# Kernel tuning notes

Hardware: AMD Instinct MI355X
Metric: run time of the kernel (lower is better)

## Reference

```python
import jax, jax.numpy as jnp
import numpy as np

N_NODES = 50000
N_EDGES = 600000
N_GRAPHS = 256


def gcn_conv(x, W, b, src, dst, n):
    # PyG GCNConv: out = D^{-1/2} (A + I) D^{-1/2} X W + b
    h = x @ W  # [N, out]
    deg = jax.ops.segment_sum(jnp.ones((src.shape[0],), h.dtype), dst, num_segments=n) + 1.0  # self-loop
    dinv = jax.lax.rsqrt(deg)  # deg >= 1 so safe
    msgs = h[src] * (dinv[src] * dinv[dst])[:, None]  # [E, out]
    agg = jax.ops.segment_sum(msgs, dst, num_segments=n)
    agg = agg + h * (dinv * dinv)[:, None]  # self-loop contribution
    return agg + b


def setup_inputs() -> dict:
    key = jax.random.key(0)
    ks = jax.random.split(key, 8)
    x = jax.random.normal(ks[0], (N_NODES, 1), dtype=jnp.float32)
    edge_index = jax.random.randint(ks[1], (2, N_EDGES), 0, N_NODES, dtype=jnp.int64)
    batch = jnp.sort(jax.random.randint(ks[2], (N_NODES,), 0, N_GRAPHS, dtype=jnp.int64))

    def glorot(k, shape):
        lim = np.sqrt(6.0 / (shape[0] + shape[1]))
        return jax.random.uniform(k, shape, jnp.float32, -lim, lim)

    return {
        "x": x,
        "W1": glorot(ks[3], (1, 64)), "b1": jnp.zeros((64,), jnp.float32),
        "W2": glorot(ks[4], (64, 128)), "b2": jnp.zeros((128,), jnp.float32),
        "W3": glorot(ks[5], (128, 64)), "b3": jnp.zeros((64,), jnp.float32),
        "lin1_w": glorot(ks[6], (64, 32)), "lin1_b": jnp.zeros((32,), jnp.float32),
        "lin2_w": glorot(ks[7], (32, 1)), "lin2_b": jnp.zeros((1,), jnp.float32),
        "edge_index": edge_index,
        "batch": batch,
    }


def reference(x, W1, b1, W2, b2, W3, b3, lin1_w, lin1_b, lin2_w, lin2_b, edge_index, batch):
    src, dst = edge_index[0], edge_index[1]
    n = x.shape[0]
    h = jax.nn.relu(gcn_conv(x, W1, b1, src, dst, n))
    h = jax.nn.relu(gcn_conv(h, W2, b2, src, dst, n))
    h = jax.nn.relu(gcn_conv(h, W3, b3, src, dst, n))
    # global_mean_pool
    sums = jax.ops.segment_sum(h, batch, num_segments=N_GRAPHS)
    cnts = jax.ops.segment_sum(jnp.ones((n,), h.dtype), batch, num_segments=N_GRAPHS)
    pooled = sums / jnp.maximum(cnts, 1.0)[:, None]  # [G, 64]
    z = jax.nn.relu(pooled @ lin1_w + lin1_b)
    return z @ lin2_w + lin2_b  # [G, 1]
```

## Files before the change

kernel.cpp:

```cpp
#include <hip/hip_runtime.h>
#include <hip/hip_fp16.h>


#define N_FEAT 64
#define POOL_SUB 16
#define SLOT 64

typedef _Float16 f16x4 __attribute__((ext_vector_type(4)));
typedef float f32x4 __attribute__((ext_vector_type(4)));

__global__ void fill_kernel(const int* __restrict__ src, const int* __restrict__ dst,
                            int* __restrict__ deg, int* __restrict__ csr, int E) {
    int e4 = (blockIdx.x * blockDim.x + threadIdx.x) * 4;
    if (e4 + 3 < E) {
        int4 sv = *(const int4*)&src[e4];
        int4 dv = *(const int4*)&dst[e4];
        int p0 = atomicAdd(&deg[dv.x], 1);
        int p1 = atomicAdd(&deg[dv.y], 1);
        int p2 = atomicAdd(&deg[dv.z], 1);
        int p3 = atomicAdd(&deg[dv.w], 1);
        csr[dv.x * SLOT + p0] = sv.x;
        csr[dv.y * SLOT + p1] = sv.y;
        csr[dv.z * SLOT + p2] = sv.z;
        csr[dv.w * SLOT + p3] = sv.w;
    } else {
        for (int e = e4; e < E; ++e) {
            int d = dst[e];
            int pos = atomicAdd(&deg[d], 1);
            csr[d * SLOT + pos] = src[e];
        }
    }
}

__global__ void prep_kernel(const int* __restrict__ deg, const float* __restrict__ x,
                            float* __restrict__ dinv, float* __restrict__ xd,
                            const float* __restrict__ W2, const float* __restrict__ W3,
                            __half* __restrict__ W2p, __half* __restrict__ W3p, int N) {
    int i = blockIdx.x * blockDim.x + threadIdx.x;
    if (i < N) {
        float dv = rsqrtf((float)deg[i] + 1.0f);
        dinv[i] = dv;
        xd[i] = x[i] * dv;
    }
    if (i < 16384) {
        if (i < 8192) {
            int ii = i & 3;
            int lane = (i >> 2) & 63;
            int blk = i >> 8;
            int k = (blk & 3) * 16 + (lane >> 4) * 4 + ii;
            int col = (blk >> 2) * 16 + (lane & 15);
            W2p[i] = __float2half(W2[k * 128 + col]);
        } else {
            int t2 = i - 8192;
            int ii = t2 & 3;
            int lane = (t2 >> 2) & 63;
            int blk = t2 >> 8;
            int k = (blk & 7) * 16 + (lane >> 4) * 4 + ii;
            int col = (blk >> 3) * 16 + (lane & 15);
            W3p[t2] = __float2half(W3[k * 64 + col]);
        }
    }
}

__global__ void sagg_gather(const int* __restrict__ deg, const int* __restrict__ csr,
                            const float* __restrict__ xd, const float* __restrict__ dinv,
                            float2* __restrict__ sd, int N) {
    int wid = (blockIdx.x * blockDim.x + threadIdx.x) >> 6;
    int lane = threadIdx.x & 63;
    int v = wid * 4 + (lane >> 4);
    int sub = lane & 15;
    if (v >= N) return;
    int dg = deg[v];
    int base = v * SLOT;
    float sum = 0.0f;
    for (int j = sub; j < dg; j += 16) sum += xd[csr[base + j]];
    #pragma unroll
    for (int off = 8; off; off >>= 1) sum += __shfl_xor(sum, off);
    if (sub == 0) {
        float dv = dinv[v];
        sd[v] = make_float2(dv * (sum + xd[v]), dv);
    }
}

__global__ void agg1_gather(const int* __restrict__ deg, const int* __restrict__ csr,
                            const float2* __restrict__ sd,
                            const float* __restrict__ W1, const float* __restrict__ b1,
                            __half* __restrict__ agg16, int N) {
    int wave = (blockIdx.x * blockDim.x + threadIdx.x) >> 6;
    int lane = threadIdx.x & 63;
    int v = wave * 2 + (lane >> 5);
    int sub = lane & 31;
    if (v >= N) return;
    float2 w  = *(const float2*)&W1[sub * 2];
    float2 bb = *(const float2*)&b1[sub * 2];
    int dg = deg[v];
    int base = v * SLOT;
    float ax = 0.0f, ay = 0.0f;
    int j = 0;
    for (; j + 3 < dg; j += 4) {
        int4 u = *(const int4*)&csr[base + j];
        float2 p0 = sd[u.x];
        float2 p1 = sd[u.y];
        float2 p2 = sd[u.z];
        float2 p3 = sd[u.w];
        ax += fmaxf(p0.x * w.x + bb.x, 0.0f) * p0.y + fmaxf(p1.x * w.x + bb.x, 0.0f) * p1.y;
        ax += fmaxf(p2.x * w.x + bb.x, 0.0f) * p2.y + fmaxf(p3.x * w.x + bb.x, 0.0f) * p3.y;
        ay += fmaxf(p0.x * w.y + bb.y, 0.0f) * p0.y + fmaxf(p1.x * w.y + bb.y, 0.0f) * p1.y;
        ay += fmaxf(p2.x * w.y + bb.y, 0.0f) * p2.y + fmaxf(p3.x * w.y + bb.y, 0.0f) * p3.y;
    }
    for (; j < dg; ++j) {
        float2 p = sd[csr[base + j]];
        ax += fmaxf(p.x * w.x + bb.x, 0.0f) * p.y;
        ay += fmaxf(p.x * w.y + bb.y, 0.0f) * p.y;
    }
    float2 pv = sd[v];
    float dv = pv.y;
    float ox = dv * ax + fmaxf(pv.x * w.x + bb.x, 0.0f) * dv * dv;
    float oy = dv * ay + fmaxf(pv.x * w.y + bb.y, 0.0f) * dv * dv;
    *(__half2*)&agg16[(size_t)v * N_FEAT + sub * 2] = __floats2half2_rn(ox, oy);
}

#define H2PAD 136
__global__ __launch_bounds__(256) void gemm12(const __half* __restrict__ A16,
                                              const __half* __restrict__ W2p,
                                              const float* __restrict__ bias2,
                                              const __half* __restrict__ W3p,
                                              const float* __restrict__ dinv,
                                              __half* __restrict__ md, int M) {
    __shared__ __half h2s[32 * H2PAD];
    int tid = threadIdx.x;
    int wave = tid >> 6, lane = tid & 63;
    int g = lane >> 4, r = lane & 15;
    int row0 = blockIdx.x * 32;

    f16x4 af[2][4];
    #pragma unroll
    for (int rt = 0; rt < 2; ++rt) {
        int row = row0 + rt * 16 + r;
        if (row >= M) row = M - 1;
        const __half* ap = A16 + (size_t)row * 64 + g * 4;
        #pragma unroll
        for (int kc = 0; kc < 4; ++kc)
            af[rt][kc] = *(const f16x4*)(ap + kc * 16);
    }

    f32x4 acc[2][2] = {};
    const f16x4* w2v = (const f16x4*)W2p;
    #pragma unroll
    for (int ctl = 0; ctl < 2; ++ctl) {
        int ct = wave * 2 + ctl;
        #pragma unroll
        for (int kc = 0; kc < 4; ++kc) {
            f16x4 bf = w2v[(ct * 4 + kc) * 64 + lane];
            acc[0][ctl] = __builtin_amdgcn_mfma_f32_16x16x16f16(af[0][kc], bf, acc[0][ctl], 0, 0, 0);
            acc[1][ctl] = __builtin_amdgcn_mfma_f32_16x16x16f16(af[1][kc], bf, acc[1][ctl], 0, 0, 0);
        }
    }
    #pragma unroll
    for (int ctl = 0; ctl < 2; ++ctl) {
        int col = (wave * 2 + ctl) * 16 + r;
        float bb = bias2[col];
        #pragma unroll
        for (int rt = 0; rt < 2; ++rt)
            #pragma unroll
            for (int i = 0; i < 4; ++i)
                h2s[(rt * 16 + g * 4 + i) * H2PAD + col] =
                    __float2half(fmaxf(acc[rt][ctl][i] + bb, 0.f));
    }
    __syncthreads();

    f32x4 acc2[2] = {};
    const f16x4* w3v = (const f16x4*)W3p;
    #pragma unroll
    for (int kc = 0; kc < 8; ++kc) {
        f16x4 bf = w3v[(wave * 8 + kc) * 64 + lane];
        #pragma unroll
        for (int rt = 0; rt < 2; ++rt) {
            f16x4 a2 = *(const f16x4*)&h2s[(rt * 16 + r) * H2PAD + kc * 16 + g * 4];
            acc2[rt] = __builtin_amdgcn_mfma_f32_16x16x16f16(a2, bf, acc2[rt], 0, 0, 0);
        }
    }
    #pragma unroll
    for (int rt = 0; rt < 2; ++rt)
        #pragma unroll
        for (int i = 0; i < 4; ++i) {
            int row = row0 + rt * 16 + g * 4 + i;
            if (row < M)
                md[(size_t)row * 64 + wave * 16 + r] = __float2half(acc2[rt][i] * dinv[row]);
        }
}

__global__ void agg3_gather(const int* __restrict__ deg, const int* __restrict__ csr,
                            const __half* __restrict__ md, const float* __restrict__ dinv,
                            float* __restrict__ agg, int N) {
    int wave = (blockIdx.x * blockDim.x + threadIdx.x) >> 6;
    int lane = threadIdx.x & 63;
    int v = wave * 4 + (lane >> 4);
    int sub = lane & 15;
    if (v >= N) return;
    const uint2* mdp = (const uint2*)md;
    int dg = deg[v];
    int base = v * SLOT;
    uint2 sv = mdp[(size_t)v * 16 + sub];
    float2 f0 = __half22float2(*(const __half2*)&sv.x);
    float2 f1 = __half22float2(*(const __half2*)&sv.y);
    float a0 = f0.x, a1 = f0.y, a2 = f1.x, a3 = f1.y;
    int j = 0;
    for (; j + 3 < dg; j += 4) {
        int4 u = *(const int4*)&csr[base + j];
        uint2 x0 = mdp[(size_t)u.x * 16 + sub];
        uint2 x1 = mdp[(size_t)u.y * 16 + sub];
        uint2 x2 = mdp[(size_t)u.z * 16 + sub];
        uint2 x3 = mdp[(size_t)u.w * 16 + sub];
        float2 p0 = __half22float2(*(const __half2*)&x0.x), q0 = __half22float2(*(const __half2*)&x0.y);
        float2 p1 = __half22float2(*(const __half2*)&x1.x), q1 = __half22float2(*(const __half2*)&x1.y);
        float2 p2 = __half22float2(*(const __half2*)&x2.x), q2 = __half22float2(*(const __half2*)&x2.y);
        float2 p3 = __half22float2(*(const __half2*)&x3.x), q3 = __half22float2(*(const __half2*)&x3.y);
        a0 += (p0.x + p1.x) + (p2.x + p3.x);
        a1 += (p0.y + p1.y) + (p2.y + p3.y);
        a2 += (q0.x + q1.x) + (q2.x + q3.x);
        a3 += (q0.y + q1.y) + (q2.y + q3.y);
    }
    for (; j < dg; ++j) {
        uint2 xv = mdp[(size_t)csr[base + j] * 16 + sub];
        float2 t0 = __half22float2(*(const __half2*)&xv.x);
        float2 t1 = __half22float2(*(const __half2*)&xv.y);
        a0 += t0.x; a1 += t0.y; a2 += t1.x; a3 += t1.y;
    }
    float dv = dinv[v];
    *(float4*)&agg[(size_t)v * N_FEAT + sub * 4] =
        make_float4(a0 * dv, a1 * dv, a2 * dv, a3 * dv);
}

__global__ void pool_kernel(const float* __restrict__ agg, const float* __restrict__ b3,
                            const int* __restrict__ batch, float* __restrict__ pooled,
                            float* __restrict__ counts, int N) {
    int wave = (blockIdx.x * blockDim.x + threadIdx.x) >> 6;
    int lane = threadIdx.x & 63;
    int start = wave * POOL_SUB;
    if (start >= N) return;
    int end = min(start + POOL_SUB, N);
    float bl = b3[lane];
    int cur = batch[start];
    float acc = 0.0f;
    float cnt = 0.0f;
    for (int i = start; i < end; ++i) {
        int g = batch[i];
        if (g != cur) {
            atomicAdd(&pooled[cur * N_FEAT + lane], acc);
            if (lane == 0) atomicAdd(&counts[cur], cnt);
            acc = 0.0f; cnt = 0.0f; cur = g;
        }
        acc += fmaxf(agg[(size_t)i * N_FEAT + lane] + bl, 0.0f);
        cnt += 1.0f;
    }
    atomicAdd(&pooled[cur * N_FEAT + lane], acc);
    if (lane == 0) atomicAdd(&counts[cur], cnt);
}

__global__ void mlp_kernel(const float* __restrict__ pooled, const float* __restrict__ counts,
                           const float* __restrict__ l1w, const float* __restrict__ l1b,
                           const float* __restrict__ l2w, const float* __restrict__ l2b,
                           float* __restrict__ out) {
    __shared__ float row[64];
    __shared__ float zs[32];
    int g = blockIdx.x;
    int l = threadIdx.x;
    float cnt = fmaxf(counts[g], 1.0f);
    row[l] = pooled[g * 64 + l] / cnt;
    __syncthreads();
    if (l < 32) {
        float z = l1b[l];
        #pragma unroll
        for (int k = 0; k < 64; ++k) z += row[k] * l1w[k * 32 + l];
        zs[l] = fmaxf(z, 0.0f);
    }
    __syncthreads();
    if (l == 0) {
        float o = l2b[0];
        #pragma unroll
        for (int j = 0; j < 32; ++j) o += zs[j] * l2w[j];
        out[g] = o;
    }
}

extern "C" void kernel_launch(void* const* d_in, const int* in_sizes, int n_in,
                              void* d_out, int out_size, void* d_ws, size_t ws_size,
                              hipStream_t stream) {
    const float* x   = (const float*)d_in[0];
    const float* W1  = (const float*)d_in[1];
    const float* b1  = (const float*)d_in[2];
    const float* W2  = (const float*)d_in[3];
    const float* b2  = (const float*)d_in[4];
    const float* W3  = (const float*)d_in[5];
    const float* b3  = (const float*)d_in[6];
    const float* l1w = (const float*)d_in[7];
    const float* l1b = (const float*)d_in[8];
    const float* l2w = (const float*)d_in[9];
    const float* l2b = (const float*)d_in[10];
    const int* ei    = (const int*)d_in[11];
    const int* batch = (const int*)d_in[12];

    int N = in_sizes[0];
    int E = in_sizes[11] / 2;
    int G = out_size;
    const int* src = ei;
    const int* dst = ei + E;

    char* wsb = (char*)d_ws;
    int*   deg      = (int*)wsb;                 wsb += (size_t)N * 4;
    float* pooled   = (float*)wsb;               wsb += (size_t)G * 64 * 4;
    float* counts   = (float*)wsb;               wsb += (size_t)G * 4;
    int*   csr      = (int*)wsb;                 wsb += (size_t)N * SLOT * 4;
    float* dinv     = (float*)wsb;               wsb += (size_t)N * 4;
    float* xd       = (float*)wsb;               wsb += (size_t)N * 4;
    float2* sd      = (float2*)wsb;              wsb += (size_t)N * 8;
    float* agg      = (float*)wsb;               wsb += (size_t)N * 64 * 4;
    __half* md      = (__half*)wsb;              wsb += (size_t)N * 64 * 2;
    __half* agg16   = (__half*)wsb;              wsb += ((size_t)N + 32) * 64 * 2;
    __half* W2p     = (__half*)wsb;              wsb += 8192 * 2;
    __half* W3p     = (__half*)wsb;              wsb += 8192 * 2;

    hipMemsetAsync(deg, 0, ((size_t)N + (size_t)G * 64 + G) * 4, stream);

    int tb = 256;
    fill_kernel<<<(E / 4 + tb - 1) / tb, tb, 0, stream>>>(src, dst, deg, csr, E);
    prep_kernel<<<(N + tb - 1) / tb, tb, 0, stream>>>(deg, x, dinv, xd, W2, W3, W2p, W3p, N);
    sagg_gather<<<((N + 3) / 4 + 3) / 4, tb, 0, stream>>>(deg, csr, xd, dinv, sd, N);
    int a1_waves = (N + 1) / 2;
    agg1_gather<<<(a1_waves + 3) / 4, tb, 0, stream>>>(deg, csr, sd, W1, b1, agg16, N);
    gemm12<<<(N + 31) / 32, tb, 0, stream>>>(agg16, W2p, b2, W3p, dinv, md, N);
    int a3_waves = (N + 3) / 4;
    agg3_gather<<<(a3_waves + 3) / 4, tb, 0, stream>>>(deg, csr, md, dinv, agg, N);
    int pool_waves = (N + POOL_SUB - 1) / POOL_SUB;
    pool_kernel<<<(pool_waves + 3) / 4, tb, 0, stream>>>(agg, b3, batch, pooled, counts, N);
    mlp_kernel<<<G, 64, 0, stream>>>(pooled, counts, l1w, l1b, l2w, l2b, (float*)d_out);
}
```

Before: 196.7 us.

## Fuse layer-3 aggregation with bias, ReLU and mean-pool via wave-level atomics

Merges the final GCN gather kernel with the pooling kernel. Bias and ReLU are applied in registers, and the four nodes handled by a wave are reduced with shuffles when they share a graph before atomically adding into the pooled buffer. This removes the N×64 fp32 agg round trip through memory and one kernel launch. In exchange it issues many more atomics per node than the old 16-node-per-wave pooling, which could cause contention on the 256 graph rows.

```diff
diff --git a/kernel.cpp b/kernel.cpp
--- a/kernel.cpp
+++ b/kernel.cpp
@@ -3,7 +3,6 @@
 
 
 #define N_FEAT 64
-#define POOL_SUB 16
 #define SLOT 64
 
 typedef _Float16 f16x4 __attribute__((ext_vector_type(4)));
@@ -190,72 +189,73 @@
         }
 }
 
-__global__ void agg3_gather(const int* __restrict__ deg, const int* __restrict__ csr,
-                            const __half* __restrict__ md, const float* __restrict__ dinv,
-                            float* __restrict__ agg, int N) {
+__global__ void agg3_pool(const int* __restrict__ deg, const int* __restrict__ csr,
+                          const __half* __restrict__ md, const float* __restrict__ dinv,
+                          const float* __restrict__ b3, const int* __restrict__ batch,
+                          float* __restrict__ pooled, float* __restrict__ counts, int N) {
     int wave = (blockIdx.x * blockDim.x + threadIdx.x) >> 6;
     int lane = threadIdx.x & 63;
-    int v = wave * 4 + (lane >> 4);
+    int qw = lane >> 4;
+    int v = wave * 4 + qw;
     int sub = lane & 15;
-    if (v >= N) return;
-    const uint2* mdp = (const uint2*)md;
-    int dg = deg[v];
-    int base = v * SLOT;
-    uint2 sv = mdp[(size_t)v * 16 + sub];
-    float2 f0 = __half22float2(*(const __half2*)&sv.x);
-    float2 f1 = __half22float2(*(const __half2*)&sv.y);
-    float a0 = f0.x, a1 = f0.y, a2 = f1.x, a3 = f1.y;
-    int j = 0;
-    for (; j + 3 < dg; j += 4) {
-        int4 u = *(const int4*)&csr[base + j];
-        uint2 x0 = mdp[(size_t)u.x * 16 + sub];
-        uint2 x1 = mdp[(size_t)u.y * 16 + sub];
-        uint2 x2 = mdp[(size_t)u.z * 16 + sub];
-        uint2 x3 = mdp[(size_t)u.w * 16 + sub];
-        float2 p0 = __half22float2(*(const __half2*)&x0.x), q0 = __half22float2(*(const __half2*)&x0.y);
-        float2 p1 = __half22float2(*(const __half2*)&x1.x), q1 = __half22float2(*(const __half2*)&x1.y);
-        float2 p2 = __half22float2(*(const __half2*)&x2.x), q2 = __half22float2(*(const __half2*)&x2.y);
-        float2 p3 = __half22float2(*(const __half2*)&x3.x), q3 = __half22float2(*(const __half2*)&x3.y);
-        a0 += (p0.x + p1.x) + (p2.x + p3.x);
-        a1 += (p0.y + p1.y) + (p2.y + p3.y);
-        a2 += (q0.x + q1.x) + (q2.x + q3.x);
-        a3 += (q0.y + q1.y) + (q2.y + q3.y);
-    }
-    for (; j < dg; ++j) {
-        uint2 xv = mdp[(size_t)csr[base + j] * 16 + sub];
-        float2 t0 = __half22float2(*(const __half2*)&xv.x);
-        float2 t1 = __half22float2(*(const __half2*)&xv.y);
-        a0 += t0.x; a1 += t0.y; a2 += t1.x; a3 += t1.y;
-    }
-    float dv = dinv[v];
-    *(float4*)&agg[(size_t)v * N_FEAT + sub * 4] =
-        make_float4(a0 * dv, a1 * dv, a2 * dv, a3 * dv);
-}
-
-__global__ void pool_kernel(const float* __restrict__ agg, const float* __restrict__ b3,
-                            const int* __restrict__ batch, float* __restrict__ pooled,
-                            float* __restrict__ counts, int N) {
-    int wave = (blockIdx.x * blockDim.x + threadIdx.x) >> 6;
-    int lane = threadIdx.x & 63;
-    int start = wave * POOL_SUB;
-    if (start >= N) return;
-    int end = min(start + POOL_SUB, N);
-    float bl = b3[lane];
-    int cur = batch[start];
-    float acc = 0.0f;
-    float cnt = 0.0f;
-    for (int i = start; i < end; ++i) {
-        int g = batch[i];
-        if (g != cur) {
-            atomicAdd(&pooled[cur * N_FEAT + lane], acc);
-            if (lane == 0) atomicAdd(&counts[cur], cnt);
-            acc = 0.0f; cnt = 0.0f; cur = g;
-        }
-        acc += fmaxf(agg[(size_t)i * N_FEAT + lane] + bl, 0.0f);
-        cnt += 1.0f;
-    }
-    atomicAdd(&pooled[cur * N_FEAT + lane], acc);
-    if (lane == 0) atomicAdd(&counts[cur], cnt);
+    bool active = v < N;
+    float a0 = 0.f, a1 = 0.f, a2 = 0.f, a3 = 0.f;
+    int g = -1;
+    if (active) {
+        g = batch[v];
+        const uint2* mdp = (const uint2*)md;
+        int dg = deg[v];
+        int base = v * SLOT;
+        uint2 sv = mdp[(size_t)v * 16 + sub];
+        float2 f0 = __half22float2(*(const __half2*)&sv.x);
+        float2 f1 = __half22float2(*(const __half2*)&sv.y);
+        a0 = f0.x; a1 = f0.y; a2 = f1.x; a3 = f1.y;
+        int j = 0;
+        for (; j + 3 < dg; j += 4) {
+            int4 u = *(const int4*)&csr[base + j];
+            uint2 x0 = mdp[(size_t)u.x * 16 + sub];
+            uint2 x1 = mdp[(size_t)u.y * 16 + sub];
+            uint2 x2 = mdp[(size_t)u.z * 16 + sub];
+            uint2 x3 = mdp[(size_t)u.w * 16 + sub];
+            float2 p0 = __half22float2(*(const __half2*)&x0.x), q0 = __half22float2(*(const __half2*)&x0.y);
+            float2 p1 = __half22float2(*(const __half2*)&x1.x), q1 = __half22float2(*(const __half2*)&x1.y);
+            float2 p2 = __half22float2(*(const __half2*)&x2.x), q2 = __half22float2(*(const __half2*)&x2.y);
+            float2 p3 = __half22float2(*(const __half2*)&x3.x), q3 = __half22float2(*(const __half2*)&x3.y);
+            a0 += (p0.x + p1.x) + (p2.x + p3.x);
+            a1 += (p0.y + p1.y) + (p2.y + p3.y);
+            a2 += (q0.x + q1.x) + (q2.x + q3.x);
+            a3 += (q0.y + q1.y) + (q2.y + q3.y);
+        }
+        for (; j < dg; ++j) {
+            uint2 xv = mdp[(size_t)csr[base + j] * 16 + sub];
+            float2 t0 = __half22float2(*(const __half2*)&xv.x);
+            float2 t1 = __half22float2(*(const __half2*)&xv.y);
+            a0 += t0.x; a1 += t0.y; a2 += t1.x; a3 += t1.y;
+        }
+        float dv = dinv[v];
+        float4 bv = *(const float4*)&b3[sub * 4];
+        a0 = fmaxf(a0 * dv + bv.x, 0.f);
+        a1 = fmaxf(a1 * dv + bv.y, 0.f);
+        a2 = fmaxf(a2 * dv + bv.z, 0.f);
+        a3 = fmaxf(a3 * dv + bv.w, 0.f);
+    }
+    int g0 = __shfl(g, 0);
+    if (__all(active && g == g0)) {
+        a0 += __shfl_xor(a0, 16); a0 += __shfl_xor(a0, 32);
+        a1 += __shfl_xor(a1, 16); a1 += __shfl_xor(a1, 32);
+        a2 += __shfl_xor(a2, 16); a2 += __shfl_xor(a2, 32);
+        a3 += __shfl_xor(a3, 16); a3 += __shfl_xor(a3, 32);
+        float myv = (qw == 0) ? a0 : (qw == 1) ? a1 : (qw == 2) ? a2 : a3;
+        atomicAdd(&pooled[g0 * N_FEAT + sub * 4 + qw], myv);
+        if (lane == 0) atomicAdd(&counts[g0], 4.0f);
+    } else if (active) {
+        float* pp = &pooled[g * N_FEAT + sub * 4];
+        atomicAdd(pp + 0, a0);
+        atomicAdd(pp + 1, a1);
+        atomicAdd(pp + 2, a2);
+        atomicAdd(pp + 3, a3);
+        if (sub == 0) atomicAdd(&counts[g], 1.0f);
+    }
 }
 
 __global__ void mlp_kernel(const float* __restrict__ pooled, const float* __restrict__ counts,
@@ -315,7 +315,6 @@
     float* dinv     = (float*)wsb;               wsb += (size_t)N * 4;
     float* xd       = (float*)wsb;               wsb += (size_t)N * 4;
     float2* sd      = (float2*)wsb;              wsb += (size_t)N * 8;
-    float* agg      = (float*)wsb;               wsb += (size_t)N * 64 * 4;
     __half* md      = (__half*)wsb;              wsb += (size_t)N * 64 * 2;
     __half* agg16   = (__half*)wsb;              wsb += ((size_t)N + 32) * 64 * 2;
     __half* W2p     = (__half*)wsb;              wsb += 8192 * 2;
@@ -331,8 +330,7 @@
     agg1_gather<<<(a1_waves + 3) / 4, tb, 0, stream>>>(deg, csr, sd, W1, b1, agg16, N);
     gemm12<<<(N + 31) / 32, tb, 0, stream>>>(agg16, W2p, b2, W3p, dinv, md, N);
     int a3_waves = (N + 3) / 4;
-    agg3_gather<<<(a3_waves + 3) / 4, tb, 0, stream>>>(deg, csr, md, dinv, agg, N);
-    int pool_waves = (N + POOL_SUB - 1) / POOL_SUB;
-    pool_kernel<<<(pool_waves + 3) / 4, tb, 0, stream>>>(agg, b3, batch, pooled, counts, N);
+    agg3_pool<<<(a3_waves + 3) / 4, tb, 0, stream>>>(deg, csr, md, dinv, b3, batch,
+                                                     pooled, counts, N);
     mlp_kernel<<<G, 64, 0, stream>>>(pooled, counts, l1w, l1b, l2w, l2b, (float*)d_out);
 }
```

After: 207.1 us. 1.05x slower.
